# Performance work log

Measured on AMD Instinct MI355X. Metric: run time of the kernel, lower is better.

The kernel has to match this reference:

```python
import jax, jax.numpy as jnp
import numpy as np

B, S, E, H = 2, 2048, 1024, 16
D = E // H  # head dim = 64
ROPE_BASE = 10000.0


def _rope(x):
    # x: [B, H, S, D]; interleaved-pair rotary embeddings (torchtune style)
    d2 = D // 2
    theta = 1.0 / (ROPE_BASE ** (jnp.arange(d2, dtype=jnp.float32) * 2.0 / D))  # [D/2]
    pos = jnp.arange(S, dtype=jnp.float32)
    ang = pos[:, None] * theta[None, :]            # [S, D/2]
    cos, sin = jnp.cos(ang), jnp.sin(ang)          # broadcast over B,H
    xr = x.reshape(B, H, S, d2, 2)
    x1, x2 = xr[..., 0], xr[..., 1]
    o1 = x1 * cos - x2 * sin
    o2 = x1 * sin + x2 * cos
    return jnp.stack([o1, o2], axis=-1).reshape(B, H, S, D)


def setup_inputs() -> dict:
    key = jax.random.key(0)
    ks = jax.random.split(key, 5)
    scale = 1.0 / np.sqrt(E)
    return {
        "x": jax.random.normal(ks[0], (B, S, E), dtype=jnp.float32),
        "Wq": jax.random.normal(ks[1], (E, E), dtype=jnp.float32) * scale,
        "Wk": jax.random.normal(ks[2], (E, E), dtype=jnp.float32) * scale,
        "Wv": jax.random.normal(ks[3], (E, E), dtype=jnp.float32) * scale,
        "Wo": jax.random.normal(ks[4], (E, E), dtype=jnp.float32) * scale,
    }


def reference(x, Wq, Wk, Wv, Wo):
    # torch Linear: y = x @ W^T
    def proj(W):
        return (x @ W.T).reshape(B, S, H, D).transpose(0, 2, 1, 3)  # [B,H,S,D]

    q = _rope(proj(Wq))
    k = _rope(proj(Wk))
    v = proj(Wv)

    attn_scale = 1.0 / np.sqrt(E)  # faithful: scales by sqrt(d_embed), not head dim
    scores = jnp.einsum('bhqd,bhkd->bhqk', q, k) * attn_scale  # [B,H,S,S]
    causal = jnp.tril(jnp.ones((S, S), dtype=bool))
    scores = jnp.where(causal, scores, -jnp.inf)
    probs = jax.nn.softmax(scores, axis=-1)
    out = jnp.einsum('bhqk,bhkd->bhqd', probs, v)  # [B,H,S,D]
    out = out.transpose(0, 2, 1, 3).reshape(B, S, E)
    return out @ Wo.T
```

## Files before the change

### kernel.cpp

```cpp
#include <hip/hip_runtime.h>
#include <hip/hip_bf16.h>
#include <math.h>

typedef __bf16 bf16;
typedef __bf16 bf16x8 __attribute__((ext_vector_type(8)));
typedef float f32x4 __attribute__((ext_vector_type(4)));

#define SEQ 2048
#define EMB 1024
#define NH  16
#define HD  64
#define NROWS 4096

#define GLOAD_LDS16(gp, lp)                                             \
    __builtin_amdgcn_global_load_lds(                                   \
        (const __attribute__((address_space(1))) void*)(gp),            \
        (__attribute__((address_space(3))) void*)(lp), 16, 0, 0)

__global__ __launch_bounds__(256) void cvt_rope_kernel(
    const float* __restrict__ x,  const float* __restrict__ Wq,
    const float* __restrict__ Wk, const float* __restrict__ Wv,
    const float* __restrict__ Wo,
    bf16* __restrict__ xb, bf16* __restrict__ Wqb, bf16* __restrict__ Wkb,
    bf16* __restrict__ Wvb, bf16* __restrict__ Wob,
    float* __restrict__ ctab, float* __restrict__ stab)
{
    int b = blockIdx.x;
    if (b >= 4096) {
        int t = (b - 4096) * 256 + threadIdx.x;
        int s = t >> 5;
        int j = t & 31;
        double freq = pow(10000.0, -(double)j / 32.0);
        double ang = (double)s * freq;
        ctab[t] = (float)cos(ang);
        stab[t] = (float)sin(ang);
        return;
    }
    const float* src; bf16* dst; int boff;
    if      (b < 2048) { src = x;  dst = xb;  boff = b;        }
    else if (b < 2560) { src = Wq; dst = Wqb; boff = b - 2048; }
    else if (b < 3072) { src = Wk; dst = Wkb; boff = b - 2560; }
    else if (b < 3584) { src = Wv; dst = Wvb; boff = b - 3072; }
    else               { src = Wo; dst = Wob; boff = b - 3584; }
    size_t off = (size_t)boff * 2048 + (size_t)threadIdx.x * 8;
    float4 f0 = *(const float4*)(src + off);
    float4 f1 = *(const float4*)(src + off + 4);
    bf16x8 v;
    v[0] = (bf16)f0.x; v[1] = (bf16)f0.y; v[2] = (bf16)f0.z; v[3] = (bf16)f0.w;
    v[4] = (bf16)f1.x; v[5] = (bf16)f1.y; v[6] = (bf16)f1.z; v[7] = (bf16)f1.w;
    *(bf16x8*)(dst + off) = v;
}

__global__ __launch_bounds__(256) void qkv_rope_kernel(
    const bf16* __restrict__ x,
    const bf16* __restrict__ Wq, const bf16* __restrict__ Wk, const bf16* __restrict__ Wv,
    const float* __restrict__ ctab, const float* __restrict__ stab,
    bf16* __restrict__ q_ws, bf16* __restrict__ kf_ws, bf16* __restrict__ vf_ws)
{
    __shared__ __align__(16) bf16 SMEM[18432];
    bf16* As = SMEM;
    bf16* Bs = SMEM + 4096;

    const int t    = threadIdx.x;
    const int lane = t & 63;
    const int wave = t >> 6;
    const int col  = lane & 15;
    const int quad = lane >> 4;

    const int nblk = blockIdx.x;
    const int m0   = blockIdx.y * 128;

    const bf16* W; int nloc;
    if (nblk < 8)       { W = Wq; nloc = nblk * 128; }
    else if (nblk < 16) { W = Wk; nloc = (nblk - 8) * 128; }
    else                { W = Wv; nloc = (nblk - 16) * 128; }

    const bf16 *ga[2], *gb[2];
#pragma unroll
    for (int j = 0; j < 2; j++) {
        int c = t + j * 256;
        ga[j] = x + (size_t)(m0 + (c >> 2)) * EMB + (c & 3) * 8;
        gb[j] = W + (size_t)(nloc + (c >> 2)) * EMB + (c & 3) * 8;
    }

    const int wm = (wave >> 1) * 64;
    const int wn = (wave & 1) * 64;

    f32x4 acc[4][4];
#pragma unroll
    for (int i = 0; i < 4; i++)
#pragma unroll
        for (int j = 0; j < 4; j++) acc[i][j] = (f32x4){0.f, 0.f, 0.f, 0.f};

    for (int kc = 0; kc < EMB; kc += 32) {
#pragma unroll
        for (int j = 0; j < 2; j++) {
            int c = t + j * 256;
            GLOAD_LDS16(ga[j] + kc, As + c * 8);
            GLOAD_LDS16(gb[j] + kc, Bs + c * 8);
        }
        __syncthreads();
        bf16x8 a[4], b[4];
#pragma unroll
        for (int mt = 0; mt < 4; mt++)
            a[mt] = *(const bf16x8*)(As + (wm + mt * 16 + col) * 32 + quad * 8);
#pragma unroll
        for (int nt = 0; nt < 4; nt++)
            b[nt] = *(const bf16x8*)(Bs + (wn + nt * 16 + col) * 32 + quad * 8);
#pragma unroll
        for (int mt = 0; mt < 4; mt++)
#pragma unroll
            for (int nt = 0; nt < 4; nt++)
                acc[mt][nt] = __builtin_amdgcn_mfma_f32_16x16x32_bf16(a[mt], b[nt], acc[mt][nt], 0, 0, 0);
        __syncthreads();
    }

    bf16* Es = SMEM + wave * 4608;

    const int n0w  = nblk * 128 + wn;
    const int m0w  = m0 + wm;
    const int bb_  = m0w >> 11;
    const int ss0  = m0w & (SEQ - 1);
    const int h    = (n0w >> 6) & 15;
    const int bh   = bb_ * NH + h;
    const int kind = (n0w < 1024) ? 0 : (n0w < 2048 ? 1 : 2);

#pragma unroll
    for (int mt = 0; mt < 4; mt++) {
#pragma unroll
        for (int nt = 0; nt < 4; nt++) {
            const int d  = nt * 16 + col;
            const int jj = d >> 1;
#pragma unroll
            for (int r = 0; r < 4; r++) {
                const int ss_l = mt * 16 + quad * 4 + r;
                float v = acc[mt][nt][r];
                if (kind < 2) {
                    float partner = __shfl_xor(v, 1, 64);
                    float c  = ctab[(ss0 + ss_l) * 32 + jj];
                    float sn = stab[(ss0 + ss_l) * 32 + jj];
                    float o = ((d & 1) == 0) ? (v * c - partner * sn)
                                             : (partner * sn + v * c);
                    if (kind == 0) {
                        Es[ss_l * 72 + d] = (bf16)(o * 0.03125f);
                    } else {
                        int eoff = ((ss_l >> 4) * 2 + (d >> 5)) * 512
                                 + ((d >> 3) & 3) * 128 + (ss_l & 15) * 8 + (d & 7);
                        Es[eoff] = (bf16)o;
                    }
                } else {
                    int eoff = ((ss_l >> 5) * 4 + (d >> 4)) * 512
                             + ((ss_l >> 3) & 3) * 128 + (d & 15) * 8 + (ss_l & 7);
                    Es[eoff] = (bf16)v;
                }
            }
        }
    }

    const int row = lane >> 3, c8 = lane & 7;
    if (kind == 0) {
        bf16* qbase = q_ws + ((size_t)bh * SEQ + ss0) * HD;
#pragma unroll
        for (int i = 0; i < 8; i++) {
            bf16x8 vv = *(const bf16x8*)&Es[(i * 8 + row) * 72 + c8 * 8];
            *(bf16x8*)(qbase + (size_t)(i * 8 + row) * HD + c8 * 8) = vv;
        }
    } else if (kind == 1) {
        bf16* kbase = kf_ws + ((size_t)bh * 128 + (ss0 >> 4)) * 1024;
#pragma unroll
        for (int i = 0; i < 8; i++) {
            bf16x8 vv = *(const bf16x8*)&Es[i * 512 + lane * 8];
            *(bf16x8*)(kbase + i * 512 + lane * 8) = vv;
        }
    } else {
        bf16* vbase = vf_ws + ((size_t)bh * 64 + (ss0 >> 5)) * 2048;
#pragma unroll
        for (int i = 0; i < 8; i++) {
            bf16x8 vv = *(const bf16x8*)&Es[i * 512 + lane * 8];
            *(bf16x8*)(vbase + i * 512 + lane * 8) = vv;
        }
    }
}

__global__ __launch_bounds__(128) void attn_kernel(
    const bf16* __restrict__ q_ws, const bf16* __restrict__ kf,
    const bf16* __restrict__ vf, bf16* __restrict__ attn_ws)
{
    __shared__ float comb_o[2][4][4][64];
    __shared__ float comb_l[2][64];

    const int lane = threadIdx.x & 63;
    const int wave = threadIdx.x >> 6;
    const int col  = lane & 15;
    const int quad = lane >> 4;

    const int qt = 63 - (int)(blockIdx.x >> 5);
    const int bh = blockIdx.x & 31;
    const int b_ = bh >> 4;
    const int h  = bh & 15;
    const int qb = qt * 32;
    const int nk = qt + 1;

    const bf16* Q  = q_ws + (size_t)bh * SEQ * HD;
    const bf16* Kf = kf + (size_t)bh * 131072;
    const bf16* Vf = vf + (size_t)bh * 131072;

    bf16x8 aq[2][2];
#pragma unroll
    for (int f = 0; f < 2; f++) {
        const bf16* qp = Q + (size_t)(qb + f * 16 + col) * HD + quad * 8;
        aq[f][0] = *(const bf16x8*)(qp);
        aq[f][1] = *(const bf16x8*)(qp + 32);
    }

    f32x4 acc_o[2][4];
#pragma unroll
    for (int f = 0; f < 2; f++)
#pragma unroll
        for (int i = 0; i < 4; i++) acc_o[f][i] = (f32x4){0.f, 0.f, 0.f, 0.f};
    float lsum[2] = {0.f, 0.f};

    int psrc[8];
#pragma unroll
    for (int j = 0; j < 8; j++)
        psrc[j] = ((((quad * 2 + (j >> 2)) & 3) << 4) | col) << 2;

    int s0 = (wave < nk) ? wave : 0;
    bf16x8 Ka[2][2], nKa[2][2];
    {
        const bf16* p = Kf + (size_t)s0 * 2048 + lane * 8;
        Ka[0][0] = *(const bf16x8*)(p);
        Ka[0][1] = *(const bf16x8*)(p + 512);
        Ka[1][0] = *(const bf16x8*)(p + 1024);
        Ka[1][1] = *(const bf16x8*)(p + 1536);
    }

    for (int s = wave; s < nk; s += 2) {
        bf16x8 Vb[4];
        {
            const bf16* p = Vf + (size_t)s * 2048 + lane * 8;
            Vb[0] = *(const bf16x8*)(p);
            Vb[1] = *(const bf16x8*)(p + 512);
            Vb[2] = *(const bf16x8*)(p + 1024);
            Vb[3] = *(const bf16x8*)(p + 1536);
        }

        f32x4 sT[2][2];
#pragma unroll
        for (int g = 0; g < 2; g++)
#pragma unroll
            for (int f = 0; f < 2; f++) {
                f32x4 z = (f32x4){0.f, 0.f, 0.f, 0.f};
                z = __builtin_amdgcn_mfma_f32_16x16x32_bf16(Ka[g][0], aq[f][0], z, 0, 0, 0);
                z = __builtin_amdgcn_mfma_f32_16x16x32_bf16(Ka[g][1], aq[f][1], z, 0, 0, 0);
                sT[g][f] = z;
            }

        {
            int sn = (s + 2 < nk) ? s + 2 : s;
            const bf16* p = Kf + (size_t)sn * 2048 + lane * 8;
            nKa[0][0] = *(const bf16x8*)(p);
            nKa[0][1] = *(const bf16x8*)(p + 512);
            nKa[1][0] = *(const bf16x8*)(p + 1024);
            nKa[1][1] = *(const bf16x8*)(p + 1536);
        }

        float p[2][2][4];
        if (s == nk - 1) {
#pragma unroll
            for (int g = 0; g < 2; g++)
#pragma unroll
                for (int f = 0; f < 2; f++) {
                    const int qg = qb + f * 16 + col;
#pragma unroll
                    for (int r = 0; r < 4; r++) {
                        int key = s * 32 + g * 16 + quad * 4 + r;
                        float e = (key <= qg) ? __expf(sT[g][f][r]) : 0.f;
                        p[g][f][r] = e;
                        lsum[f] += e;
                    }
                }
        } else {
#pragma unroll
            for (int g = 0; g < 2; g++)
#pragma unroll
                for (int f = 0; f < 2; f++)
#pragma unroll
                    for (int r = 0; r < 4; r++) {
                        float e = __expf(sT[g][f][r]);
                        p[g][f][r] = e;
                        lsum[f] += e;
                    }
        }

#pragma unroll
        for (int f = 0; f < 2; f++) {
            unsigned int pk[4];
#pragma unroll
            for (int r = 0; r < 4; r++) {
                unsigned int lo = __builtin_bit_cast(unsigned short, (bf16)p[0][f][r]);
                unsigned int hi = __builtin_bit_cast(unsigned short, (bf16)p[1][f][r]);
                pk[r] = (hi << 16) | lo;
            }
            bf16x8 a_p;
#pragma unroll
            for (int j = 0; j < 8; j++) {
                unsigned int g = (unsigned int)__builtin_amdgcn_ds_bpermute(psrc[j], (int)pk[j & 3]);
                unsigned short bits = (quad < 2) ? (unsigned short)(g & 0xffff)
                                                 : (unsigned short)(g >> 16);
                a_p[j] = __builtin_bit_cast(bf16, bits);
            }
#pragma unroll
            for (int nt = 0; nt < 4; nt++)
                acc_o[f][nt] = __builtin_amdgcn_mfma_f32_16x16x32_bf16(a_p, Vb[nt], acc_o[f][nt], 0, 0, 0);
        }

        Ka[0][0] = nKa[0][0]; Ka[0][1] = nKa[0][1];
        Ka[1][0] = nKa[1][0]; Ka[1][1] = nKa[1][1];
    }

    if (wave == 1) {
#pragma unroll
        for (int f = 0; f < 2; f++) {
            comb_l[f][lane] = lsum[f];
#pragma unroll
            for (int nt = 0; nt < 4; nt++)
#pragma unroll
                for (int r = 0; r < 4; r++)
                    comb_o[f][nt][r][lane] = acc_o[f][nt][r];
        }
    }
    __syncthreads();

    if (wave == 0) {
#pragma unroll
        for (int f = 0; f < 2; f++) {
            lsum[f] += comb_l[f][lane];
#pragma unroll
            for (int nt = 0; nt < 4; nt++)
#pragma unroll
                for (int r = 0; r < 4; r++)
                    acc_o[f][nt][r] += comb_o[f][nt][r][lane];
        }

#pragma unroll
        for (int f = 0; f < 2; f++) {
            lsum[f] += __shfl_xor(lsum[f], 16, 64);
            lsum[f] += __shfl_xor(lsum[f], 32, 64);
        }
#pragma unroll
        for (int f = 0; f < 2; f++)
#pragma unroll
            for (int r = 0; r < 4; r++) {
                float l_r = __shfl(lsum[f], quad * 4 + r, 64);
                float inv = 1.0f / l_r;
                int q = qb + f * 16 + quad * 4 + r;
                bf16* orow = attn_ws + (size_t)(b_ * SEQ + q) * EMB + h * HD;
#pragma unroll
                for (int nt = 0; nt < 4; nt++)
                    orow[nt * 16 + col] = (bf16)(acc_o[f][nt][r] * inv);
            }
    }
}

__global__ __launch_bounds__(256) void oproj_kernel(
    const bf16* __restrict__ attn_ws, const bf16* __restrict__ Wo,
    float* __restrict__ out)
{
    __shared__ __align__(16) char SM[36864];
    bf16* As = (bf16*)SM;
    bf16* Bs = (bf16*)(SM + 8192);

    const int t    = threadIdx.x;
    const int lane = t & 63;
    const int wave = t >> 6;
    const int col  = lane & 15;
    const int quad = lane >> 4;

    const int n0 = blockIdx.x * 64;
    const int m0 = blockIdx.y * 128;

    const bf16 *ga[2], *gb;
#pragma unroll
    for (int j = 0; j < 2; j++) {
        int c = t + j * 256;
        ga[j] = attn_ws + (size_t)(m0 + (c >> 2)) * EMB + (c & 3) * 8;
    }
    gb = Wo + (size_t)(n0 + (t >> 2)) * EMB + (t & 3) * 8;

    const int wm = (wave >> 1) * 64;
    const int wn = (wave & 1) * 32;

    f32x4 acc[4][2];
#pragma unroll
    for (int i = 0; i < 4; i++)
#pragma unroll
        for (int j = 0; j < 2; j++) acc[i][j] = (f32x4){0.f, 0.f, 0.f, 0.f};

    for (int kc = 0; kc < EMB; kc += 32) {
#pragma unroll
        for (int j = 0; j < 2; j++) {
            int c = t + j * 256;
            GLOAD_LDS16(ga[j] + kc, As + c * 8);
        }
        GLOAD_LDS16(gb + kc, Bs + t * 8);
        __syncthreads();
        bf16x8 a[4], b[2];
#pragma unroll
        for (int mt = 0; mt < 4; mt++)
            a[mt] = *(const bf16x8*)(As + (wm + mt * 16 + col) * 32 + quad * 8);
#pragma unroll
        for (int nt = 0; nt < 2; nt++)
            b[nt] = *(const bf16x8*)(Bs + (wn + nt * 16 + col) * 32 + quad * 8);
#pragma unroll
        for (int mt = 0; mt < 4; mt++)
#pragma unroll
            for (int nt = 0; nt < 2; nt++)
                acc[mt][nt] = __builtin_amdgcn_mfma_f32_16x16x32_bf16(a[mt], b[nt], acc[mt][nt], 0, 0, 0);
        __syncthreads();
    }

    float* Os = (float*)(SM + (size_t)wave * 9216);
#pragma unroll
    for (int mt = 0; mt < 4; mt++)
#pragma unroll
        for (int nt = 0; nt < 2; nt++)
#pragma unroll
            for (int r = 0; r < 4; r++)
                Os[(mt * 16 + quad * 4 + r) * 36 + nt * 16 + col] = acc[mt][nt][r];

    const int row = lane >> 3, c8 = lane & 7;
    float* obase = out + (size_t)(m0 + wm) * EMB + n0 + wn;
#pragma unroll
    for (int i = 0; i < 8; i++) {
        float4 vv = *(const float4*)&Os[(i * 8 + row) * 36 + c8 * 4];
        *(float4*)(obase + (size_t)(i * 8 + row) * EMB + c8 * 4) = vv;
    }
}

extern "C" void kernel_launch(void* const* d_in, const int* in_sizes, int n_in,
                              void* d_out, int out_size, void* d_ws, size_t ws_size,
                              hipStream_t stream) {
    const float* x  = (const float*)d_in[0];
    const float* Wq = (const float*)d_in[1];
    const float* Wk = (const float*)d_in[2];
    const float* Wv = (const float*)d_in[3];
    const float* Wo = (const float*)d_in[4];
    float* out = (float*)d_out;

    char* ws = (char*)d_ws;
    bf16* q_ws    = (bf16*)(ws);
    bf16* kf_ws   = (bf16*)(ws + (8u  << 20));
    bf16* vf_ws   = (bf16*)(ws + (16u << 20));
    bf16* xb      = (bf16*)(ws + (24u << 20));
    bf16* attn_ws = (bf16*)(ws + (24u << 20));
    bf16* Wqb     = (bf16*)(ws + (32u << 20));
    bf16* Wkb     = (bf16*)(ws + (34u << 20));
    bf16* Wvb     = (bf16*)(ws + (36u << 20));
    bf16* Wob     = (bf16*)(ws + (38u << 20));
    float* ctab   = (float*)(ws + (40u << 20));
    float* stab   = ctab + SEQ * 32;

    hipLaunchKernelGGL(cvt_rope_kernel, dim3(4352), dim3(256), 0, stream,
                       x, Wq, Wk, Wv, Wo, xb, Wqb, Wkb, Wvb, Wob, ctab, stab);
    hipLaunchKernelGGL(qkv_rope_kernel, dim3(24, 32), dim3(256), 0, stream,
                       xb, Wqb, Wkb, Wvb, ctab, stab, q_ws, kf_ws, vf_ws);
    hipLaunchKernelGGL(attn_kernel, dim3(2048), dim3(128), 0, stream,
                       q_ws, kf_ws, vf_ws, attn_ws);
    hipLaunchKernelGGL(oproj_kernel, dim3(16, 32), dim3(256), 0, stream,
                       attn_ws, Wob, out);
}
```

Before: 180.7 us.

## Split attention key blocks across four waves with bf16 LDS partial combine

The attention kernel now runs four waves per block instead of two, each wave handling every fourth 32-key tile, so each query tile's key loop is spread across more waves. The partial outputs are combined through shared memory as bf16 (to limit LDS size), and each wave then finalises one 16-column slice of the head output, so all waves share the epilogue. This cuts per-wave serial work for long causal rows and raises wave-level parallelism, at the cost of more LDS traffic, higher register and LDS pressure per block, and rounding the partial outputs to bf16 before the sum.

```diff
diff --git a/kernel.cpp b/kernel.cpp
--- a/kernel.cpp
+++ b/kernel.cpp
@@ -182,12 +182,12 @@
     }
 }
 
-__global__ __launch_bounds__(128) void attn_kernel(
+__global__ __launch_bounds__(256) void attn_kernel(
     const bf16* __restrict__ q_ws, const bf16* __restrict__ kf,
     const bf16* __restrict__ vf, bf16* __restrict__ attn_ws)
 {
-    __shared__ float comb_o[2][4][4][64];
-    __shared__ float comb_l[2][64];
+    __shared__ bf16  parts_o[4][2][4][4][64];
+    __shared__ float parts_l[4][2][64];
 
     const int lane = threadIdx.x & 63;
     const int wave = threadIdx.x >> 6;
@@ -235,7 +235,7 @@
         Ka[1][1] = *(const bf16x8*)(p + 1536);
     }
 
-    for (int s = wave; s < nk; s += 2) {
+    for (int s = wave; s < nk; s += 4) {
         bf16x8 Vb[4];
         {
             const bf16* p = Vf + (size_t)s * 2048 + lane * 8;
@@ -257,7 +257,7 @@
             }
 
         {
-            int sn = (s + 2 < nk) ? s + 2 : s;
+            int sn = (s + 4 < nk) ? s + 4 : s;
             const bf16* p = Kf + (size_t)sn * 2048 + lane * 8;
             nKa[0][0] = *(const bf16x8*)(p);
             nKa[0][1] = *(const bf16x8*)(p + 512);
@@ -319,48 +319,42 @@
         Ka[1][0] = nKa[1][0]; Ka[1][1] = nKa[1][1];
     }
 
-    if (wave == 1) {
-#pragma unroll
-        for (int f = 0; f < 2; f++) {
-            comb_l[f][lane] = lsum[f];
-#pragma unroll
-            for (int nt = 0; nt < 4; nt++)
-#pragma unroll
-                for (int r = 0; r < 4; r++)
-                    comb_o[f][nt][r][lane] = acc_o[f][nt][r];
-        }
+#pragma unroll
+    for (int f = 0; f < 2; f++) {
+        parts_l[wave][f][lane] = lsum[f];
+#pragma unroll
+        for (int nt = 0; nt < 4; nt++)
+#pragma unroll
+            for (int r = 0; r < 4; r++)
+                parts_o[wave][f][nt][r][lane] = (bf16)acc_o[f][nt][r];
     }
     __syncthreads();
 
-    if (wave == 0) {
-#pragma unroll
-        for (int f = 0; f < 2; f++) {
-            lsum[f] += comb_l[f][lane];
-#pragma unroll
-            for (int nt = 0; nt < 4; nt++)
-#pragma unroll
-                for (int r = 0; r < 4; r++)
-                    acc_o[f][nt][r] += comb_o[f][nt][r][lane];
-        }
-
-#pragma unroll
-        for (int f = 0; f < 2; f++) {
-            lsum[f] += __shfl_xor(lsum[f], 16, 64);
-            lsum[f] += __shfl_xor(lsum[f], 32, 64);
-        }
-#pragma unroll
-        for (int f = 0; f < 2; f++)
-#pragma unroll
-            for (int r = 0; r < 4; r++) {
-                float l_r = __shfl(lsum[f], quad * 4 + r, 64);
-                float inv = 1.0f / l_r;
-                int q = qb + f * 16 + quad * 4 + r;
-                bf16* orow = attn_ws + (size_t)(b_ * SEQ + q) * EMB + h * HD;
-#pragma unroll
-                for (int nt = 0; nt < 4; nt++)
-                    orow[nt * 16 + col] = (bf16)(acc_o[f][nt][r] * inv);
-            }
-    }
+    float linv[2][4];
+#pragma unroll
+    for (int f = 0; f < 2; f++) {
+        float lf = parts_l[0][f][lane] + parts_l[1][f][lane]
+                 + parts_l[2][f][lane] + parts_l[3][f][lane];
+        lf += __shfl_xor(lf, 16, 64);
+        lf += __shfl_xor(lf, 32, 64);
+#pragma unroll
+        for (int r = 0; r < 4; r++)
+            linv[f][r] = 1.0f / __shfl(lf, quad * 4 + r, 64);
+    }
+
+    const int nt = wave;
+#pragma unroll
+    for (int f = 0; f < 2; f++)
+#pragma unroll
+        for (int r = 0; r < 4; r++) {
+            float o = (float)parts_o[0][f][nt][r][lane]
+                    + (float)parts_o[1][f][nt][r][lane]
+                    + (float)parts_o[2][f][nt][r][lane]
+                    + (float)parts_o[3][f][nt][r][lane];
+            int q = qb + f * 16 + quad * 4 + r;
+            attn_ws[(size_t)(b_ * SEQ + q) * EMB + h * HD + nt * 16 + col]
+                = (bf16)(o * linv[f][r]);
+        }
 }
 
 __global__ __launch_bounds__(256) void oproj_kernel(
@@ -465,7 +459,7 @@
                        x, Wq, Wk, Wv, Wo, xb, Wqb, Wkb, Wvb, Wob, ctab, stab);
     hipLaunchKernelGGL(qkv_rope_kernel, dim3(24, 32), dim3(256), 0, stream,
                        xb, Wqb, Wkb, Wvb, ctab, stab, q_ws, kf_ws, vf_ws);
-    hipLaunchKernelGGL(attn_kernel, dim3(2048), dim3(128), 0, stream,
+    hipLaunchKernelGGL(attn_kernel, dim3(2048), dim3(256), 0, stream,
                        q_ws, kf_ws, vf_ws, attn_ws);
     hipLaunchKernelGGL(oproj_kernel, dim3(16, 32), dim3(256), 0, stream,
                        attn_ws, Wob, out);
```

After: 182.6 us. About the same (+1.1%).

## Double K-step per barrier in projection GEMMs and use exp2 softmax

Applied to the files above, without the earlier changes.

Both projection GEMMs (QKV and output) now load two 32-wide K slices into shared memory per iteration and compute both before the next barrier. This halves the number of __syncthreads per K sweep and lets more global-to-LDS loads be in flight at once. Separately, the Q pre-scale now folds in log2(e), so the attention softmax can use exp2f instead of __expf. The cost is roughly twice the LDS footprint for the tiles, which still fits inside the existing buffers.

```diff
diff --git a/kernel.cpp b/kernel.cpp
--- a/kernel.cpp
+++ b/kernel.cpp
@@ -16,6 +16,8 @@
     __builtin_amdgcn_global_load_lds(                                   \
         (const __attribute__((address_space(1))) void*)(gp),            \
         (__attribute__((address_space(3))) void*)(lp), 16, 0, 0)
+
+#define QSCALE 0.045084439f
 
 __global__ __launch_bounds__(256) void cvt_rope_kernel(
     const float* __restrict__ x,  const float* __restrict__ Wq,
@@ -59,7 +61,7 @@
 {
     __shared__ __align__(16) bf16 SMEM[18432];
     bf16* As = SMEM;
-    bf16* Bs = SMEM + 4096;
+    bf16* Bs = SMEM + 8192;
 
     const int t    = threadIdx.x;
     const int lane = t & 63;
@@ -92,26 +94,31 @@
 #pragma unroll
         for (int j = 0; j < 4; j++) acc[i][j] = (f32x4){0.f, 0.f, 0.f, 0.f};
 
-    for (int kc = 0; kc < EMB; kc += 32) {
-#pragma unroll
-        for (int j = 0; j < 2; j++) {
-            int c = t + j * 256;
-            GLOAD_LDS16(ga[j] + kc, As + c * 8);
-            GLOAD_LDS16(gb[j] + kc, Bs + c * 8);
-        }
+    for (int kc = 0; kc < EMB; kc += 64) {
+#pragma unroll
+        for (int p = 0; p < 2; p++)
+#pragma unroll
+            for (int j = 0; j < 2; j++) {
+                int c = t + j * 256;
+                GLOAD_LDS16(ga[j] + kc + p * 32, As + p * 4096 + c * 8);
+                GLOAD_LDS16(gb[j] + kc + p * 32, Bs + p * 4096 + c * 8);
+            }
         __syncthreads();
-        bf16x8 a[4], b[4];
-#pragma unroll
-        for (int mt = 0; mt < 4; mt++)
-            a[mt] = *(const bf16x8*)(As + (wm + mt * 16 + col) * 32 + quad * 8);
-#pragma unroll
-        for (int nt = 0; nt < 4; nt++)
-            b[nt] = *(const bf16x8*)(Bs + (wn + nt * 16 + col) * 32 + quad * 8);
-#pragma unroll
-        for (int mt = 0; mt < 4; mt++)
+#pragma unroll
+        for (int p = 0; p < 2; p++) {
+            bf16x8 a[4], b[4];
+#pragma unroll
+            for (int mt = 0; mt < 4; mt++)
+                a[mt] = *(const bf16x8*)(As + p * 4096 + (wm + mt * 16 + col) * 32 + quad * 8);
 #pragma unroll
             for (int nt = 0; nt < 4; nt++)
-                acc[mt][nt] = __builtin_amdgcn_mfma_f32_16x16x32_bf16(a[mt], b[nt], acc[mt][nt], 0, 0, 0);
+                b[nt] = *(const bf16x8*)(Bs + p * 4096 + (wn + nt * 16 + col) * 32 + quad * 8);
+#pragma unroll
+            for (int mt = 0; mt < 4; mt++)
+#pragma unroll
+                for (int nt = 0; nt < 4; nt++)
+                    acc[mt][nt] = __builtin_amdgcn_mfma_f32_16x16x32_bf16(a[mt], b[nt], acc[mt][nt], 0, 0, 0);
+        }
         __syncthreads();
     }
 
@@ -142,7 +149,7 @@
                     float o = ((d & 1) == 0) ? (v * c - partner * sn)
                                              : (partner * sn + v * c);
                     if (kind == 0) {
-                        Es[ss_l * 72 + d] = (bf16)(o * 0.03125f);
+                        Es[ss_l * 72 + d] = (bf16)(o * QSCALE);
                     } else {
                         int eoff = ((ss_l >> 4) * 2 + (d >> 5)) * 512
                                  + ((d >> 3) & 3) * 128 + (ss_l & 15) * 8 + (d & 7);
@@ -275,7 +282,7 @@
 #pragma unroll
                     for (int r = 0; r < 4; r++) {
                         int key = s * 32 + g * 16 + quad * 4 + r;
-                        float e = (key <= qg) ? __expf(sT[g][f][r]) : 0.f;
+                        float e = (key <= qg) ? exp2f(sT[g][f][r]) : 0.f;
                         p[g][f][r] = e;
                         lsum[f] += e;
                     }
@@ -287,7 +294,7 @@
                 for (int f = 0; f < 2; f++)
 #pragma unroll
                     for (int r = 0; r < 4; r++) {
-                        float e = __expf(sT[g][f][r]);
+                        float e = exp2f(sT[g][f][r]);
                         p[g][f][r] = e;
                         lsum[f] += e;
                     }
@@ -369,7 +376,7 @@
 {
     __shared__ __align__(16) char SM[36864];
     bf16* As = (bf16*)SM;
-    bf16* Bs = (bf16*)(SM + 8192);
+    bf16* Bs = (bf16*)(SM + 16384);
 
     const int t    = threadIdx.x;
     const int lane = t & 63;
@@ -397,26 +404,32 @@
 #pragma unroll
         for (int j = 0; j < 2; j++) acc[i][j] = (f32x4){0.f, 0.f, 0.f, 0.f};
 
-    for (int kc = 0; kc < EMB; kc += 32) {
-#pragma unroll
-        for (int j = 0; j < 2; j++) {
-            int c = t + j * 256;
-            GLOAD_LDS16(ga[j] + kc, As + c * 8);
-        }
-        GLOAD_LDS16(gb + kc, Bs + t * 8);
+    for (int kc = 0; kc < EMB; kc += 64) {
+#pragma unroll
+        for (int p = 0; p < 2; p++) {
+#pragma unroll
+            for (int j = 0; j < 2; j++) {
+                int c = t + j * 256;
+                GLOAD_LDS16(ga[j] + kc + p * 32, As + p * 4096 + c * 8);
+            }
+            GLOAD_LDS16(gb + kc + p * 32, Bs + p * 2048 + t * 8);
+        }
         __syncthreads();
-        bf16x8 a[4], b[2];
-#pragma unroll
-        for (int mt = 0; mt < 4; mt++)
-            a[mt] = *(const bf16x8*)(As + (wm + mt * 16 + col) * 32 + quad * 8);
-#pragma unroll
-        for (int nt = 0; nt < 2; nt++)
-            b[nt] = *(const bf16x8*)(Bs + (wn + nt * 16 + col) * 32 + quad * 8);
-#pragma unroll
-        for (int mt = 0; mt < 4; mt++)
+#pragma unroll
+        for (int p = 0; p < 2; p++) {
+            bf16x8 a[4], b[2];
+#pragma unroll
+            for (int mt = 0; mt < 4; mt++)
+                a[mt] = *(const bf16x8*)(As + p * 4096 + (wm + mt * 16 + col) * 32 + quad * 8);
 #pragma unroll
             for (int nt = 0; nt < 2; nt++)
-                acc[mt][nt] = __builtin_amdgcn_mfma_f32_16x16x32_bf16(a[mt], b[nt], acc[mt][nt], 0, 0, 0);
+                b[nt] = *(const bf16x8*)(Bs + p * 2048 + (wn + nt * 16 + col) * 32 + quad * 8);
+#pragma unroll
+            for (int mt = 0; mt < 4; mt++)
+#pragma unroll
+                for (int nt = 0; nt < 2; nt++)
+                    acc[mt][nt] = __builtin_amdgcn_mfma_f32_16x16x32_bf16(a[mt], b[nt], acc[mt][nt], 0, 0, 0);
+        }
         __syncthreads();
     }
 
```

Result: slower. 206.1 us (+14.1%).
